# Optimization experiments

Measured on AMD Instinct MI355X. Metric: run time of the kernel, lower is better.

## Reference

```python
import jax, jax.numpy as jnp
import numpy as np

B, L, T_ENC = 64, 128, 256
C_IN, UNITS, OUT = 256, 512, 128  # state_size == motor_size == UNITS (fully-connected wiring)


def _make_params(key):
    ks = jax.random.split(key, 12)
    def rn(k, shape):
        return jax.random.normal(k, shape, dtype=jnp.float32) / np.sqrt(shape[-1])
    cat = C_IN + UNITS  # CfC cell concatenates [input, hx]
    p = {}
    p["W_dec"] = rn(ks[0], (UNITS, 2 * UNITS))                 # fcn_dec, no bias
    p["W_enc"] = rn(ks[1], (UNITS, UNITS)); p["b_enc"] = jnp.zeros((UNITS,), jnp.float32)
    p["w_score"] = rn(ks[2], (1, UNITS))                       # fcn_score Linear(H,1,bias=False)
    p["W_yattn"] = rn(ks[3], (C_IN, UNITS + C_IN)); p["b_yattn"] = jnp.zeros((C_IN,), jnp.float32)
    p["W_ih"] = rn(ks[4], (4 * UNITS, C_IN)); p["b_ih"] = jnp.zeros((4 * UNITS,), jnp.float32)
    p["W_hh"] = rn(ks[5], (4 * UNITS, UNITS))                  # ncps LSTMCell recurrent map has no bias
    p["W_ff1"] = rn(ks[6], (UNITS, cat)); p["b_ff1"] = jnp.zeros((UNITS,), jnp.float32)
    p["W_ff2"] = rn(ks[7], (UNITS, cat)); p["b_ff2"] = jnp.zeros((UNITS,), jnp.float32)
    p["W_ta"] = rn(ks[8], (UNITS, cat)); p["b_ta"] = jnp.zeros((UNITS,), jnp.float32)
    p["W_tb"] = rn(ks[9], (UNITS, cat)); p["b_tb"] = jnp.zeros((UNITS,), jnp.float32)
    p["W_o1"] = rn(ks[10], (UNITS, 2 * UNITS)); p["b_o1"] = jnp.zeros((UNITS,), jnp.float32)
    p["W_o2"] = rn(ks[11], (OUT, UNITS)); p["b_o2"] = jnp.zeros((OUT,), jnp.float32)
    return p


def setup_inputs() -> dict:
    key = jax.random.key(0)
    k1, k2, k3 = jax.random.split(key, 3)
    inp = {
        "x": jax.random.normal(k1, (B, L, C_IN), dtype=jnp.float32),
        "h_en": jax.random.normal(k2, (B, T_ENC, UNITS), dtype=jnp.float32),
    }
    inp.update(_make_params(k3))
    return inp


def _forward(x, h_en, W_dec, W_enc, b_enc, w_score, W_yattn, b_yattn,
             W_ih, b_ih, W_hh, W_ff1, b_ff1, W_ff2, b_ff2,
             W_ta, b_ta, W_tb, b_tb, W_o1, b_o1, W_o2, b_o2):
    Bsz = x.shape[0]
    # fcn_enc applied once outside the time loop (as in the source)
    proj_enc = jnp.einsum('btm,hm->bth', h_en, W_enc) + b_enc  # (B,T_enc,H)
    ts = 1.0  # timespans=None

    def step(carry, xt):
        h, cst, _, _ = carry
        # attention over encoder states
        proj_dec = jnp.concatenate([h, cst], axis=1) @ W_dec.T               # (B,H)
        e = jnp.einsum('bth,h->bt', jnp.tanh(proj_dec[:, None, :] + proj_enc), w_score[0])
        score = jax.nn.softmax(e, axis=1)                                    # softmax over T_enc
        c = jnp.einsum('bt,btm->bm', score, h_en)                            # context (B,M)
        x_hat = jnp.concatenate([xt, c], axis=1) @ W_yattn.T + b_yattn       # (B,C_IN)
        # ncps LSTMCell (forget-gate bias +1)
        z = x_hat @ W_ih.T + b_ih + h @ W_hh.T
        i_, ig, fg, og = jnp.split(z, 4, axis=1)
        new_c = cst * jax.nn.sigmoid(fg + 1.0) + jnp.tanh(i_) * jax.nn.sigmoid(ig)
        h_lstm = jnp.tanh(new_c) * jax.nn.sigmoid(og)
        # WiredCfCCell: single fully-connected layer, mode='default', no backbone
        xx = jnp.concatenate([x_hat, h_lstm], axis=1)                        # (B,C_IN+H)
        ff1 = jnp.tanh(xx @ W_ff1.T + b_ff1)
        ff2 = jnp.tanh(xx @ W_ff2.T + b_ff2)
        t_interp = jax.nn.sigmoid((xx @ W_ta.T + b_ta) * ts + (xx @ W_tb.T + b_tb))
        new_h = ff1 * (1.0 - t_interp) + t_interp * ff2                      # new h_state == h_out
        return (new_h, new_c, new_h, c), None

    h0 = jnp.zeros((Bsz, UNITS), x.dtype)
    init = (h0, h0, h0, jnp.zeros((Bsz, UNITS), x.dtype))
    (h_state, c_state, h_out, c_last), _ = jax.lax.scan(step, init, jnp.swapaxes(x, 0, 1))
    hid = jax.nn.leaky_relu(jnp.concatenate([h_out, c_last], axis=1) @ W_o1.T + b_o1)
    out = hid @ W_o2.T + b_o2
    return out, h_state, c_state


def reference(x, h_en, W_dec, W_enc, b_enc, w_score, W_yattn, b_yattn,
              W_ih, b_ih, W_hh, W_ff1, b_ff1, W_ff2, b_ff2,
              W_ta, b_ta, W_tb, b_tb, W_o1, b_o1, W_o2, b_o2):
    return _forward(x, h_en, W_dec, W_enc, b_enc, w_score, W_yattn, b_yattn,
                    W_ih, b_ih, W_hh, W_ff1, b_ff1, W_ff2, b_ff2,
                    W_ta, b_ta, W_tb, b_tb, W_o1, b_o1, W_o2, b_o2)
```

## Files before the change

### kernel.cpp

```cpp
#include <hip/hip_runtime.h>


constexpr int BSZ  = 64;
constexpr int LSEQ = 128;
constexpr int TENC = 256;
constexpr int CIN  = 256;
constexpr int HU   = 512;
constexpr int ODIM = 128;
constexpr int NBLK = 256;
constexpr int KBIG = 1 << 30;

typedef unsigned long long ull;

struct Params {
  const float *x, *h_en, *W_dec, *W_enc, *b_enc, *w_score, *W_yattn, *b_yattn;
  const float *W_ih, *b_ih, *W_hh;
  const float *W_ff1, *b_ff1, *W_ff2, *b_ff2, *W_ta, *b_ta, *W_tb, *b_tb;
  const float *W_o1, *b_o1, *W_o2, *b_o2;
  float *out;
  float *pe;
  float *pd_part;
  float *e_buf;
  float *ctx;
  float *xhat;
  float *hlstm;
  float *h_buf;
  float *c_buf;
  float *hid;
  unsigned *bar;
  unsigned *flags;
};

__device__ __forceinline__ float frcp_(float x) { return __builtin_amdgcn_rcpf(x); }
__device__ __forceinline__ float ftanh_(float x) {
  return 1.0f - 2.0f * frcp_(1.0f + __expf(2.0f * x));
}
__device__ __forceinline__ float fsig_(float x) {
  return frcp_(1.0f + __expf(-x));
}

__device__ __forceinline__ float ld_c(const float* p) {
  return __hip_atomic_load(p, __ATOMIC_RELAXED, __HIP_MEMORY_SCOPE_AGENT);
}
__device__ __forceinline__ float2 ld_c2(const float* p) {
  union { ull u; float2 f; } c;
  c.u = __hip_atomic_load((const ull*)p, __ATOMIC_RELAXED, __HIP_MEMORY_SCOPE_AGENT);
  return c.f;
}
__device__ __forceinline__ void st_c(float* p, float v) {
  __hip_atomic_store(p, v, __ATOMIC_RELAXED, __HIP_MEMORY_SCOPE_AGENT);
}

__device__ __forceinline__ void gridbar(unsigned* bar, unsigned* flags, unsigned gen) {
  __syncthreads();
  const int t = threadIdx.x;
  if (t == 0) {
    asm volatile("s_waitcnt vmcnt(0) lgkmcnt(0)" ::: "memory");
    __hip_atomic_store(flags + blockIdx.x * 16, gen,
                       __ATOMIC_RELAXED, __HIP_MEMORY_SCOPE_AGENT);
  }
  if (blockIdx.x == 0) {
    while (__hip_atomic_load(flags + t * 16, __ATOMIC_RELAXED,
                             __HIP_MEMORY_SCOPE_AGENT) < gen)
      __builtin_amdgcn_s_sleep(1);
    __syncthreads();
    if (t == 0)
      __hip_atomic_store(bar, gen, __ATOMIC_RELAXED, __HIP_MEMORY_SCOPE_AGENT);
  }
  if (t == 0) {
    while (__hip_atomic_load(bar, __ATOMIC_RELAXED,
                             __HIP_MEMORY_SCOPE_AGENT) < gen)
      __builtin_amdgcn_s_sleep(1);
  }
  __syncthreads();
}

__device__ __forceinline__ void stage128(
    float (*As)[132], float (*Ws)[132], int arows, int wrows,
    const float* const* wr0, const float* const* wr1, int splitW,
    const float* A0, int lda0, bool s0,
    const float* A1, int lda1, bool s1, int splitA, int kb)
{
  const int t = threadIdx.x;
  const float* A; int lda; bool sc;
  if (kb < splitA) { A = A0 + kb;            lda = lda0; sc = s0; }
  else             { A = A1 + (kb - splitA); lda = lda1; sc = s1; }
  if (sc) {
    for (int idx = t; idx < arows * 64; idx += 256) {
      int r = idx >> 6, kd = (idx & 63) << 1;
      *(float2*)&As[r][kd] = ld_c2(A + r * lda + kd);
    }
  } else {
    for (int idx = t; idx < arows * 32; idx += 256) {
      int r = idx >> 5, kq = (idx & 31) << 2;
      *(float4*)&As[r][kq] = *(const float4*)(A + r * lda + kq);
    }
  }
  const float* const* wr; int ko;
  if (kb < splitW) { wr = wr0; ko = kb; } else { wr = wr1; ko = kb - splitW; }
  for (int idx = t; idx < wrows * 32; idx += 256) {
    int c = idx >> 5, kq = (idx & 31) << 2;
    *(float4*)&Ws[c][kq] = *(const float4*)(wr[c] + ko + kq);
  }
}

__device__ __forceinline__ void gemm64x16(
    float (*As)[132], float (*Ws)[132],
    const float* const* wr0, const float* const* wr1, int splitW, const float* biasS,
    const float* A0, int lda0, bool s0, const float* A1, int lda1, bool s1, int splitA,
    int kbase, int klen, float (&acc)[2][2], int& b0o, int& c0o)
{
  const int t = threadIdx.x;
  const int c0 = (t & 7) * 2;
  const int b0 = (t >> 3) * 2;
  __syncthreads();
  acc[0][0] = biasS[c0]; acc[0][1] = biasS[c0 + 1];
  acc[1][0] = biasS[c0]; acc[1][1] = biasS[c0 + 1];
  const int ns = klen >> 7;
  for (int s = 0; s < ns; ++s) {
    stage128(As, Ws, 64, 16, wr0, wr1, splitW, A0, lda0, s0, A1, lda1, s1, splitA,
             kbase + (s << 7));
    __syncthreads();
#pragma unroll
    for (int k4 = 0; k4 < 32; ++k4) {
      float4 w0 = *(float4*)&Ws[c0][k4 << 2];
      float4 w1 = *(float4*)&Ws[c0 + 1][k4 << 2];
#pragma unroll
      for (int i = 0; i < 2; ++i) {
        float4 a = *(float4*)&As[b0 + i][k4 << 2];
        acc[i][0] = fmaf(a.x, w0.x, acc[i][0]);
        acc[i][0] = fmaf(a.y, w0.y, acc[i][0]);
        acc[i][0] = fmaf(a.z, w0.z, acc[i][0]);
        acc[i][0] = fmaf(a.w, w0.w, acc[i][0]);
        acc[i][1] = fmaf(a.x, w1.x, acc[i][1]);
        acc[i][1] = fmaf(a.y, w1.y, acc[i][1]);
        acc[i][1] = fmaf(a.z, w1.z, acc[i][1]);
        acc[i][1] = fmaf(a.w, w1.w, acc[i][1]);
      }
    }
    __syncthreads();
  }
  b0o = b0; c0o = c0;
}

__device__ __forceinline__ void gemm32x16(
    float (*As)[132], float (*Ws)[132],
    const float* const* wr0, const float* const* wr1, int splitW, const float* biasS,
    const float* A0, int lda0, bool s0, const float* A1, int lda1, bool s1, int splitA,
    int kbase, int klen, float (&acc)[2], int& b0o, int& c0o)
{
  const int t = threadIdx.x;
  const int c0 = (t & 7) * 2;
  const int b0 = t >> 3;
  __syncthreads();
  acc[0] = biasS[c0]; acc[1] = biasS[c0 + 1];
  const int ns = klen >> 7;
  for (int s = 0; s < ns; ++s) {
    stage128(As, Ws, 32, 16, wr0, wr1, splitW, A0, lda0, s0, A1, lda1, s1, splitA,
             kbase + (s << 7));
    __syncthreads();
#pragma unroll
    for (int k4 = 0; k4 < 32; ++k4) {
      float4 w0 = *(float4*)&Ws[c0][k4 << 2];
      float4 w1 = *(float4*)&Ws[c0 + 1][k4 << 2];
      float4 a  = *(float4*)&As[b0][k4 << 2];
      acc[0] = fmaf(a.x, w0.x, acc[0]);
      acc[0] = fmaf(a.y, w0.y, acc[0]);
      acc[0] = fmaf(a.z, w0.z, acc[0]);
      acc[0] = fmaf(a.w, w0.w, acc[0]);
      acc[1] = fmaf(a.x, w1.x, acc[1]);
      acc[1] = fmaf(a.y, w1.y, acc[1]);
      acc[1] = fmaf(a.z, w1.z, acc[1]);
      acc[1] = fmaf(a.w, w1.w, acc[1]);
    }
    __syncthreads();
  }
  b0o = b0; c0o = c0;
}

__device__ __forceinline__ void gemm64x32(
    float (*As)[132], float (*Ws)[132],
    const float* const* wr0, const float* biasS,
    const float* A0, int lda0, int klen, float (&acc)[2][4], int& b0o, int& c0o)
{
  const int t = threadIdx.x;
  const int c0 = (t & 7) * 4;
  const int b0 = (t >> 3) * 2;
  __syncthreads();
#pragma unroll
  for (int i = 0; i < 2; ++i)
#pragma unroll
    for (int j = 0; j < 4; ++j) acc[i][j] = biasS[c0 + j];
  const int ns = klen >> 7;
  for (int s = 0; s < ns; ++s) {
    stage128(As, Ws, 64, 32, wr0, wr0, KBIG, A0, lda0, false, A0, lda0, false, KBIG,
             s << 7);
    __syncthreads();
#pragma unroll
    for (int k4 = 0; k4 < 32; ++k4) {
      float4 w0 = *(float4*)&Ws[c0][k4 << 2];
      float4 w1 = *(float4*)&Ws[c0 + 1][k4 << 2];
      float4 w2 = *(float4*)&Ws[c0 + 2][k4 << 2];
      float4 w3 = *(float4*)&Ws[c0 + 3][k4 << 2];
#pragma unroll
      for (int i = 0; i < 2; ++i) {
        float4 a = *(float4*)&As[b0 + i][k4 << 2];
        acc[i][0] = fmaf(a.x, w0.x, acc[i][0]); acc[i][0] = fmaf(a.y, w0.y, acc[i][0]);
        acc[i][0] = fmaf(a.z, w0.z, acc[i][0]); acc[i][0] = fmaf(a.w, w0.w, acc[i][0]);
        acc[i][1] = fmaf(a.x, w1.x, acc[i][1]); acc[i][1] = fmaf(a.y, w1.y, acc[i][1]);
        acc[i][1] = fmaf(a.z, w1.z, acc[i][1]); acc[i][1] = fmaf(a.w, w1.w, acc[i][1]);
        acc[i][2] = fmaf(a.x, w2.x, acc[i][2]); acc[i][2] = fmaf(a.y, w2.y, acc[i][2]);
        acc[i][2] = fmaf(a.z, w2.z, acc[i][2]); acc[i][2] = fmaf(a.w, w2.w, acc[i][2]);
        acc[i][3] = fmaf(a.x, w3.x, acc[i][3]); acc[i][3] = fmaf(a.y, w3.y, acc[i][3]);
        acc[i][3] = fmaf(a.z, w3.z, acc[i][3]); acc[i][3] = fmaf(a.w, w3.w, acc[i][3]);
      }
    }
    __syncthreads();
  }
  b0o = b0; c0o = c0;
}

__launch_bounds__(256)
__global__ void cfc_kernel(Params P) {
  __shared__ float As[64][132];
  __shared__ float Ws[32][132];
  __shared__ const float* wr0[32];
  __shared__ const float* wr1[32];
  __shared__ float biasS[32];
  __shared__ float misc[1088];

  const int t = threadIdx.x;
  unsigned gen = 1;

  for (int job = blockIdx.x; job < 4096 + 32; job += NBLK) {
    if (job < 4096) {
      int rt = job >> 4, ct = job & 15;
      if (t < 32) {
        wr0[t] = P.W_enc + (ct * 32 + t) * HU;
        biasS[t] = P.b_enc[ct * 32 + t];
      }
      float acc[2][4]; int b0, c0;
      gemm64x32(As, Ws, wr0, biasS, P.h_en + rt * 64 * HU, HU, 512, acc, b0, c0);
      float* outp = P.pe + rt * 64 * HU + ct * 32;
#pragma unroll
      for (int i = 0; i < 2; ++i)
#pragma unroll
        for (int j = 0; j < 4; ++j)
          outp[(b0 + i) * HU + c0 + j] = acc[i][j];
    } else {
      int idx = job - 4096;
      float* base = (idx < 16 ? P.h_buf : P.c_buf) + (idx & 15) * 2048;
      for (int i = t; i < 2048; i += 256) st_c(base + i, 0.f);
    }
  }
  __builtin_amdgcn_fence(__ATOMIC_RELEASE, "agent");
  gridbar(P.bar, P.flags, gen++);

  for (int step = 0; step < LSEQ; ++step) {
    const float* xt = P.x + step * CIN;

    {
      int ut = blockIdx.x & 31, ks = blockIdx.x >> 5;
      if (t < 16) {
        wr0[t] = P.W_dec + (ut * 16 + t) * 1024;
        wr1[t] = wr0[t];
        biasS[t] = 0.f;
      }
      float acc[2][2]; int b0, c0;
      gemm64x16(As, Ws, wr0, wr1, KBIG, biasS,
                P.h_buf, HU, true, P.c_buf, HU, true, 512,
                ks * 128, 128, acc, b0, c0);
      float* outp = P.pd_part + ks * (BSZ * HU) + ut * 16;
      st_c(outp + b0 * HU + c0,           acc[0][0]);
      st_c(outp + b0 * HU + c0 + 1,       acc[0][1]);
      st_c(outp + (b0 + 1) * HU + c0,     acc[1][0]);
      st_c(outp + (b0 + 1) * HU + c0 + 1, acc[1][1]);
    }
    gridbar(P.bar, P.flags, gen++);

    {
      int b = blockIdx.x >> 2, tq = blockIdx.x & 3;
      float* pds = misc;
      float* wsc = misc + 520;
      __syncthreads();
      for (int h = t; h < HU; h += 256) {
        float s = 0.f;
#pragma unroll
        for (int p8 = 0; p8 < 8; ++p8) s += ld_c(P.pd_part + p8 * (BSZ * HU) + b * HU + h);
        int hs = h + (h >> 7);
        pds[hs] = s;
        wsc[hs] = P.w_score[h];
      }
      __syncthreads();
      int q = t & 3, tt = tq * 64 + (t >> 2);
      const float* per = P.pe + (b * TENC + tt) * HU + q * 128;
      float acc = 0.f;
      for (int h4 = 0; h4 < 32; ++h4) {
        float4 pv = *(const float4*)(per + h4 * 4);
        int hbs = q * 129 + h4 * 4;
        acc += wsc[hbs + 0] * ftanh_(pds[hbs + 0] + pv.x);
        acc += wsc[hbs + 1] * ftanh_(pds[hbs + 1] + pv.y);
        acc += wsc[hbs + 2] * ftanh_(pds[hbs + 2] + pv.z);
        acc += wsc[hbs + 3] * ftanh_(pds[hbs + 3] + pv.w);
      }
      acc += __shfl_xor(acc, 1);
      acc += __shfl_xor(acc, 2);
      if (q == 0) st_c(P.e_buf + b * TENC + tt, acc);
    }
    gridbar(P.bar, P.flags, gen++);

    {
      int b = blockIdx.x >> 2, mq = blockIdx.x & 3;
      float* es = misc;
      float* red = misc + 512;
      float v = ld_c(P.e_buf + b * TENC + t);
      float m = v;
#pragma unroll
      for (int o = 1; o < 64; o <<= 1) m = fmaxf(m, __shfl_xor(m, o));
      int wid = t >> 6;
      if ((t & 63) == 0) red[wid] = m;
      __syncthreads();
      m = fmaxf(fmaxf(red[0], red[1]), fmaxf(red[2], red[3]));
      float p = __expf(v - m);
      float s = p;
#pragma unroll
      for (int o = 1; o < 64; o <<= 1) s += __shfl_xor(s, o);
      if ((t & 63) == 0) red[4 + wid] = s;
      __syncthreads();
      float sum = (red[4] + red[5]) + (red[6] + red[7]);
      es[t] = p * frcp_(sum);
      __syncthreads();
      if (t < 128) {
        int mcol = mq * 128 + t;
        const float* hb = P.h_en + b * TENC * HU + mcol;
        float a0 = 0.f, a1 = 0.f, a2 = 0.f, a3 = 0.f;
        for (int tt = 0; tt < TENC; tt += 4) {
          a0 = fmaf(es[tt + 0], hb[(tt + 0) * HU], a0);
          a1 = fmaf(es[tt + 1], hb[(tt + 1) * HU], a1);
          a2 = fmaf(es[tt + 2], hb[(tt + 2) * HU], a2);
          a3 = fmaf(es[tt + 3], hb[(tt + 3) * HU], a3);
        }
        st_c(P.ctx + b * HU + mcol, (a0 + a1) + (a2 + a3));
      }
    }
    gridbar(P.bar, P.flags, gen++);

    if (blockIdx.x < 16) {
      int ot = blockIdx.x;
      if (t < 16) {
        wr0[t] = P.W_yattn + (ot * 16 + t) * 768;
        wr1[t] = wr0[t];
        biasS[t] = P.b_yattn[ot * 16 + t];
      }
      float acc[2][2]; int b0, c0;
      gemm64x16(As, Ws, wr0, wr1, KBIG, biasS,
                xt, LSEQ * CIN, false, P.ctx, HU, true, 256,
                0, 768, acc, b0, c0);
      float* outp = P.xhat + ot * 16;
      st_c(outp + b0 * CIN + c0,           acc[0][0]);
      st_c(outp + b0 * CIN + c0 + 1,       acc[0][1]);
      st_c(outp + (b0 + 1) * CIN + c0,     acc[1][0]);
      st_c(outp + (b0 + 1) * CIN + c0 + 1, acc[1][1]);
    }
    gridbar(P.bar, P.flags, gen++);

    {
      int bt = blockIdx.x & 1, jq = blockIdx.x >> 1;
      int j0 = jq * 4, rowbase = bt * 32;
      if (t < 16) {
        int jj = t >> 2, g = t & 3;
        int r = g * 512 + j0 + jj;
        wr0[t] = P.W_ih + r * 256;
        wr1[t] = P.W_hh + r * 512;
        biasS[t] = P.b_ih[r];
      }
      float acc[2]; int b0, c0;
      gemm32x16(As, Ws, wr0, wr1, 256, biasS,
                P.xhat + rowbase * CIN, CIN, true,
                P.h_buf + rowbase * HU, HU, true, 256,
                0, 768, acc, b0, c0);
      float* zs = misc;
      zs[b0 * 16 + c0] = acc[0];
      zs[b0 * 16 + c0 + 1] = acc[1];
      __syncthreads();
      if (t < 128) {
        int b = t >> 2, jj = t & 3;
        int gb = rowbase + b, j = j0 + jj;
        float i_ = zs[b * 16 + jj * 4 + 0];
        float ig = zs[b * 16 + jj * 4 + 1];
        float fg = zs[b * 16 + jj * 4 + 2];
        float og = zs[b * 16 + jj * 4 + 3];
        float cold = ld_c(P.c_buf + gb * HU + j);
        float cn = cold * fsig_(fg + 1.0f) + ftanh_(i_) * fsig_(ig);
        st_c(P.c_buf + gb * HU + j, cn);
        st_c(P.hlstm + gb * HU + j, ftanh_(cn) * fsig_(og));
      }
    }
    gridbar(P.bar, P.flags, gen++);

    {
      int bt = blockIdx.x & 1, jq = blockIdx.x >> 1;
      int j0 = jq * 4, rowbase = bt * 32;
      if (t < 16) {
        int jj = t >> 2, m = t & 3;
        const float* Wm = (m == 0) ? P.W_ff1 : (m == 1) ? P.W_ff2 : (m == 2) ? P.W_ta : P.W_tb;
        const float* bm = (m == 0) ? P.b_ff1 : (m == 1) ? P.b_ff2 : (m == 2) ? P.b_ta : P.b_tb;
        wr0[t] = Wm + (j0 + jj) * 768;
        wr1[t] = wr0[t];
        biasS[t] = bm[j0 + jj];
      }
      float acc[2]; int b0, c0;
      gemm32x16(As, Ws, wr0, wr1, KBIG, biasS,
                P.xhat + rowbase * CIN, CIN, true,
                P.hlstm + rowbase * HU, HU, true, 256,
                0, 768, acc, b0, c0);
      float* es2 = misc;
      es2[b0 * 16 + c0] = acc[0];
      es2[b0 * 16 + c0 + 1] = acc[1];
      __syncthreads();
      if (t < 128) {
        int b = t >> 2, jj = t & 3;
        int gb = rowbase + b, j = j0 + jj;
        float ff1 = ftanh_(es2[b * 16 + jj * 4 + 0]);
        float ff2 = ftanh_(es2[b * 16 + jj * 4 + 1]);
        float ta  = es2[b * 16 + jj * 4 + 2];
        float tb  = es2[b * 16 + jj * 4 + 3];
        float ti = fsig_(ta + tb);
        st_c(P.h_buf + gb * HU + j, ff1 * (1.0f - ti) + ti * ff2);
      }
    }
    gridbar(P.bar, P.flags, gen++);
  }

  if (blockIdx.x < 32) {
    int ut = blockIdx.x;
    if (t < 16) {
      wr0[t] = P.W_o1 + (ut * 16 + t) * 1024;
      wr1[t] = wr0[t];
      biasS[t] = P.b_o1[ut * 16 + t];
    }
    float acc[2][2]; int b0, c0;
    gemm64x16(As, Ws, wr0, wr1, KBIG, biasS,
              P.h_buf, HU, true, P.ctx, HU, true, 512,
              0, 1024, acc, b0, c0);
    float* outp = P.hid + ut * 16;
#pragma unroll
    for (int i = 0; i < 2; ++i)
#pragma unroll
      for (int j = 0; j < 2; ++j) {
        float v = acc[i][j];
        st_c(outp + (b0 + i) * HU + c0 + j, v > 0.f ? v : 0.01f * v);
      }
  }
  gridbar(P.bar, P.flags, gen++);

  {
    int job = blockIdx.x;
    if (job < 8) {
      if (t < 16) {
        wr0[t] = P.W_o2 + (job * 16 + t) * HU;
        wr1[t] = wr0[t];
        biasS[t] = P.b_o2[job * 16 + t];
      }
      float acc[2][2]; int b0, c0;
      gemm64x16(As, Ws, wr0, wr1, KBIG, biasS,
                P.hid, HU, true, P.hid, HU, true, KBIG,
                0, 512, acc, b0, c0);
      float* outp = P.out + job * 16;
      outp[b0 * ODIM + c0] = acc[0][0];
      outp[b0 * ODIM + c0 + 1] = acc[0][1];
      outp[(b0 + 1) * ODIM + c0] = acc[1][0];
      outp[(b0 + 1) * ODIM + c0 + 1] = acc[1][1];
    } else if (job < 40) {
      int idx = job - 8;
      const float* src = (idx < 16 ? P.h_buf : P.c_buf) + (idx & 15) * 2048;
      float* dst = P.out + BSZ * ODIM + (idx < 16 ? 0 : BSZ * HU) + (idx & 15) * 2048;
      for (int i = t; i < 1024; i += 256) {
        float2 f = ld_c2(src + 2 * i);
        *(float2*)(dst + 2 * i) = f;
      }
    }
  }
}

extern "C" void kernel_launch(void* const* d_in, const int* in_sizes, int n_in,
                              void* d_out, int out_size, void* d_ws, size_t ws_size,
                              hipStream_t stream) {
  (void)in_sizes; (void)n_in; (void)out_size; (void)ws_size;
  Params P;
  P.x       = (const float*)d_in[0];
  P.h_en    = (const float*)d_in[1];
  P.W_dec   = (const float*)d_in[2];
  P.W_enc   = (const float*)d_in[3];
  P.b_enc   = (const float*)d_in[4];
  P.w_score = (const float*)d_in[5];
  P.W_yattn = (const float*)d_in[6];
  P.b_yattn = (const float*)d_in[7];
  P.W_ih    = (const float*)d_in[8];
  P.b_ih    = (const float*)d_in[9];
  P.W_hh    = (const float*)d_in[10];
  P.W_ff1   = (const float*)d_in[11];
  P.b_ff1   = (const float*)d_in[12];
  P.W_ff2   = (const float*)d_in[13];
  P.b_ff2   = (const float*)d_in[14];
  P.W_ta    = (const float*)d_in[15];
  P.b_ta    = (const float*)d_in[16];
  P.W_tb    = (const float*)d_in[17];
  P.b_tb    = (const float*)d_in[18];
  P.W_o1    = (const float*)d_in[19];
  P.b_o1    = (const float*)d_in[20];
  P.W_o2    = (const float*)d_in[21];
  P.b_o2    = (const float*)d_in[22];
  P.out     = (float*)d_out;

  float* ws = (float*)d_ws;
  size_t off = 0;
  P.pe      = ws + off; off += (size_t)BSZ * TENC * HU;
  P.pd_part = ws + off; off += (size_t)8 * BSZ * HU;
  P.e_buf   = ws + off; off += (size_t)BSZ * TENC;
  P.ctx     = ws + off; off += (size_t)BSZ * HU;
  P.xhat    = ws + off; off += (size_t)BSZ * CIN;
  P.hlstm   = ws + off; off += (size_t)BSZ * HU;
  P.h_buf   = ws + off; off += (size_t)BSZ * HU;
  P.c_buf   = ws + off; off += (size_t)BSZ * HU;
  P.hid     = ws + off; off += (size_t)BSZ * HU;
  P.bar     = (unsigned*)(ws + off); off += 16;
  P.flags   = (unsigned*)(ws + off);

  (void)hipMemsetAsync((void*)P.bar, 0, 64 + 256 * 64, stream);

  hipLaunchKernelGGL(cfc_kernel, dim3(NBLK), dim3(256), 0, stream, P);
}
```

Before: 17.95 ms.

## Restructure persistent CfC kernel GEMM stages with split-K and more blocks per phase

Replaces the generic staged GEMM helpers with inline LDS tiling and small dot-product microkernels, and splits the y-attention GEMM across K into partial buffers summed by the consumer. Output and head GEMMs now use 32-row batch tiles so more blocks participate. Coherent atomic loads are replaced by plain vector loads, with an acquire fence added after the grid barrier. The encoder-projection job order is also changed. The goal is lower per-step latency in the sequential loop, at the cost of relying on the fence for memory visibility.

```diff
diff --git a/kernel.cpp b/kernel.cpp
--- a/kernel.cpp
+++ b/kernel.cpp
@@ -8,9 +8,6 @@
 constexpr int HU   = 512;
 constexpr int ODIM = 128;
 constexpr int NBLK = 256;
-constexpr int KBIG = 1 << 30;
-
-typedef unsigned long long ull;
 
 struct Params {
   const float *x, *h_en, *W_dec, *W_enc, *b_enc, *w_score, *W_yattn, *b_yattn;
@@ -22,7 +19,7 @@
   float *pd_part;
   float *e_buf;
   float *ctx;
-  float *xhat;
+  float *xh_part;
   float *hlstm;
   float *h_buf;
   float *c_buf;
@@ -39,14 +36,6 @@
   return frcp_(1.0f + __expf(-x));
 }
 
-__device__ __forceinline__ float ld_c(const float* p) {
-  return __hip_atomic_load(p, __ATOMIC_RELAXED, __HIP_MEMORY_SCOPE_AGENT);
-}
-__device__ __forceinline__ float2 ld_c2(const float* p) {
-  union { ull u; float2 f; } c;
-  c.u = __hip_atomic_load((const ull*)p, __ATOMIC_RELAXED, __HIP_MEMORY_SCOPE_AGENT);
-  return c.f;
-}
 __device__ __forceinline__ void st_c(float* p, float v) {
   __hip_atomic_store(p, v, __ATOMIC_RELAXED, __HIP_MEMORY_SCOPE_AGENT);
 }
@@ -71,177 +60,115 @@
     while (__hip_atomic_load(bar, __ATOMIC_RELAXED,
                              __HIP_MEMORY_SCOPE_AGENT) < gen)
       __builtin_amdgcn_s_sleep(1);
+    __builtin_amdgcn_fence(__ATOMIC_ACQUIRE, "agent");
   }
   __syncthreads();
 }
 
-__device__ __forceinline__ void stage128(
-    float (*As)[132], float (*Ws)[132], int arows, int wrows,
-    const float* const* wr0, const float* const* wr1, int splitW,
-    const float* A0, int lda0, bool s0,
-    const float* A1, int lda1, bool s1, int splitA, int kb)
-{
-  const int t = threadIdx.x;
-  const float* A; int lda; bool sc;
-  if (kb < splitA) { A = A0 + kb;            lda = lda0; sc = s0; }
-  else             { A = A1 + (kb - splitA); lda = lda1; sc = s1; }
-  if (sc) {
-    for (int idx = t; idx < arows * 64; idx += 256) {
-      int r = idx >> 6, kd = (idx & 63) << 1;
-      *(float2*)&As[r][kd] = ld_c2(A + r * lda + kd);
-    }
-  } else {
-    for (int idx = t; idx < arows * 32; idx += 256) {
-      int r = idx >> 5, kq = (idx & 31) << 2;
-      *(float4*)&As[r][kq] = *(const float4*)(A + r * lda + kq);
-    }
-  }
-  const float* const* wr; int ko;
-  if (kb < splitW) { wr = wr0; ko = kb; } else { wr = wr1; ko = kb - splitW; }
-  for (int idx = t; idx < wrows * 32; idx += 256) {
-    int c = idx >> 5, kq = (idx & 31) << 2;
-    *(float4*)&Ws[c][kq] = *(const float4*)(wr[c] + ko + kq);
-  }
-}
-
-__device__ __forceinline__ void gemm64x16(
-    float (*As)[132], float (*Ws)[132],
-    const float* const* wr0, const float* const* wr1, int splitW, const float* biasS,
-    const float* A0, int lda0, bool s0, const float* A1, int lda1, bool s1, int splitA,
-    int kbase, int klen, float (&acc)[2][2], int& b0o, int& c0o)
-{
-  const int t = threadIdx.x;
-  const int c0 = (t & 7) * 2;
-  const int b0 = (t >> 3) * 2;
-  __syncthreads();
-  acc[0][0] = biasS[c0]; acc[0][1] = biasS[c0 + 1];
-  acc[1][0] = biasS[c0]; acc[1][1] = biasS[c0 + 1];
-  const int ns = klen >> 7;
-  for (int s = 0; s < ns; ++s) {
-    stage128(As, Ws, 64, 16, wr0, wr1, splitW, A0, lda0, s0, A1, lda1, s1, splitA,
-             kbase + (s << 7));
-    __syncthreads();
-#pragma unroll
-    for (int k4 = 0; k4 < 32; ++k4) {
-      float4 w0 = *(float4*)&Ws[c0][k4 << 2];
-      float4 w1 = *(float4*)&Ws[c0 + 1][k4 << 2];
-#pragma unroll
-      for (int i = 0; i < 2; ++i) {
-        float4 a = *(float4*)&As[b0 + i][k4 << 2];
-        acc[i][0] = fmaf(a.x, w0.x, acc[i][0]);
-        acc[i][0] = fmaf(a.y, w0.y, acc[i][0]);
-        acc[i][0] = fmaf(a.z, w0.z, acc[i][0]);
-        acc[i][0] = fmaf(a.w, w0.w, acc[i][0]);
-        acc[i][1] = fmaf(a.x, w1.x, acc[i][1]);
-        acc[i][1] = fmaf(a.y, w1.y, acc[i][1]);
-        acc[i][1] = fmaf(a.z, w1.z, acc[i][1]);
-        acc[i][1] = fmaf(a.w, w1.w, acc[i][1]);
-      }
-    }
-    __syncthreads();
-  }
-  b0o = b0; c0o = c0;
-}
-
-__device__ __forceinline__ void gemm32x16(
-    float (*As)[132], float (*Ws)[132],
-    const float* const* wr0, const float* const* wr1, int splitW, const float* biasS,
-    const float* A0, int lda0, bool s0, const float* A1, int lda1, bool s1, int splitA,
-    int kbase, int klen, float (&acc)[2], int& b0o, int& c0o)
-{
-  const int t = threadIdx.x;
-  const int c0 = (t & 7) * 2;
-  const int b0 = t >> 3;
-  __syncthreads();
-  acc[0] = biasS[c0]; acc[1] = biasS[c0 + 1];
-  const int ns = klen >> 7;
-  for (int s = 0; s < ns; ++s) {
-    stage128(As, Ws, 32, 16, wr0, wr1, splitW, A0, lda0, s0, A1, lda1, s1, splitA,
-             kbase + (s << 7));
-    __syncthreads();
-#pragma unroll
-    for (int k4 = 0; k4 < 32; ++k4) {
-      float4 w0 = *(float4*)&Ws[c0][k4 << 2];
-      float4 w1 = *(float4*)&Ws[c0 + 1][k4 << 2];
-      float4 a  = *(float4*)&As[b0][k4 << 2];
-      acc[0] = fmaf(a.x, w0.x, acc[0]);
-      acc[0] = fmaf(a.y, w0.y, acc[0]);
-      acc[0] = fmaf(a.z, w0.z, acc[0]);
-      acc[0] = fmaf(a.w, w0.w, acc[0]);
-      acc[1] = fmaf(a.x, w1.x, acc[1]);
-      acc[1] = fmaf(a.y, w1.y, acc[1]);
-      acc[1] = fmaf(a.z, w1.z, acc[1]);
-      acc[1] = fmaf(a.w, w1.w, acc[1]);
-    }
-    __syncthreads();
-  }
-  b0o = b0; c0o = c0;
-}
-
-__device__ __forceinline__ void gemm64x32(
-    float (*As)[132], float (*Ws)[132],
-    const float* const* wr0, const float* biasS,
-    const float* A0, int lda0, int klen, float (&acc)[2][4], int& b0o, int& c0o)
-{
-  const int t = threadIdx.x;
-  const int c0 = (t & 7) * 4;
-  const int b0 = (t >> 3) * 2;
-  __syncthreads();
-#pragma unroll
-  for (int i = 0; i < 2; ++i)
-#pragma unroll
-    for (int j = 0; j < 4; ++j) acc[i][j] = biasS[c0 + j];
-  const int ns = klen >> 7;
-  for (int s = 0; s < ns; ++s) {
-    stage128(As, Ws, 64, 32, wr0, wr0, KBIG, A0, lda0, false, A0, lda0, false, KBIG,
-             s << 7);
-    __syncthreads();
-#pragma unroll
-    for (int k4 = 0; k4 < 32; ++k4) {
-      float4 w0 = *(float4*)&Ws[c0][k4 << 2];
-      float4 w1 = *(float4*)&Ws[c0 + 1][k4 << 2];
-      float4 w2 = *(float4*)&Ws[c0 + 2][k4 << 2];
-      float4 w3 = *(float4*)&Ws[c0 + 3][k4 << 2];
-#pragma unroll
-      for (int i = 0; i < 2; ++i) {
-        float4 a = *(float4*)&As[b0 + i][k4 << 2];
-        acc[i][0] = fmaf(a.x, w0.x, acc[i][0]); acc[i][0] = fmaf(a.y, w0.y, acc[i][0]);
-        acc[i][0] = fmaf(a.z, w0.z, acc[i][0]); acc[i][0] = fmaf(a.w, w0.w, acc[i][0]);
-        acc[i][1] = fmaf(a.x, w1.x, acc[i][1]); acc[i][1] = fmaf(a.y, w1.y, acc[i][1]);
-        acc[i][1] = fmaf(a.z, w1.z, acc[i][1]); acc[i][1] = fmaf(a.w, w1.w, acc[i][1]);
-        acc[i][2] = fmaf(a.x, w2.x, acc[i][2]); acc[i][2] = fmaf(a.y, w2.y, acc[i][2]);
-        acc[i][2] = fmaf(a.z, w2.z, acc[i][2]); acc[i][2] = fmaf(a.w, w2.w, acc[i][2]);
-        acc[i][3] = fmaf(a.x, w3.x, acc[i][3]); acc[i][3] = fmaf(a.y, w3.y, acc[i][3]);
-        acc[i][3] = fmaf(a.z, w3.z, acc[i][3]); acc[i][3] = fmaf(a.w, w3.w, acc[i][3]);
-      }
-    }
-    __syncthreads();
-  }
-  b0o = b0; c0o = c0;
+__device__ __forceinline__ void dot2x2(const float* A0, const float* A1,
+                                       const float* W0, const float* W1,
+                                       int nk4, float (&acc)[2][2]) {
+#pragma unroll 8
+  for (int k4 = 0; k4 < nk4; ++k4) {
+    float4 w0 = *(const float4*)(W0 + (k4 << 2));
+    float4 w1 = *(const float4*)(W1 + (k4 << 2));
+    float4 a0 = *(const float4*)(A0 + (k4 << 2));
+    float4 a1 = *(const float4*)(A1 + (k4 << 2));
+    acc[0][0] = fmaf(a0.x, w0.x, acc[0][0]); acc[0][0] = fmaf(a0.y, w0.y, acc[0][0]);
+    acc[0][0] = fmaf(a0.z, w0.z, acc[0][0]); acc[0][0] = fmaf(a0.w, w0.w, acc[0][0]);
+    acc[0][1] = fmaf(a0.x, w1.x, acc[0][1]); acc[0][1] = fmaf(a0.y, w1.y, acc[0][1]);
+    acc[0][1] = fmaf(a0.z, w1.z, acc[0][1]); acc[0][1] = fmaf(a0.w, w1.w, acc[0][1]);
+    acc[1][0] = fmaf(a1.x, w0.x, acc[1][0]); acc[1][0] = fmaf(a1.y, w0.y, acc[1][0]);
+    acc[1][0] = fmaf(a1.z, w0.z, acc[1][0]); acc[1][0] = fmaf(a1.w, w0.w, acc[1][0]);
+    acc[1][1] = fmaf(a1.x, w1.x, acc[1][1]); acc[1][1] = fmaf(a1.y, w1.y, acc[1][1]);
+    acc[1][1] = fmaf(a1.z, w1.z, acc[1][1]); acc[1][1] = fmaf(a1.w, w1.w, acc[1][1]);
+  }
+}
+
+__device__ __forceinline__ void dot1x2(const float* A0,
+                                       const float* W0, const float* W1,
+                                       int nk4, float (&acc)[2]) {
+#pragma unroll 8
+  for (int k4 = 0; k4 < nk4; ++k4) {
+    float4 w0 = *(const float4*)(W0 + (k4 << 2));
+    float4 w1 = *(const float4*)(W1 + (k4 << 2));
+    float4 a  = *(const float4*)(A0 + (k4 << 2));
+    acc[0] = fmaf(a.x, w0.x, acc[0]); acc[0] = fmaf(a.y, w0.y, acc[0]);
+    acc[0] = fmaf(a.z, w0.z, acc[0]); acc[0] = fmaf(a.w, w0.w, acc[0]);
+    acc[1] = fmaf(a.x, w1.x, acc[1]); acc[1] = fmaf(a.y, w1.y, acc[1]);
+    acc[1] = fmaf(a.z, w1.z, acc[1]); acc[1] = fmaf(a.w, w1.w, acc[1]);
+  }
+}
+
+__device__ __forceinline__ void dot2x4(const float* A0, const float* A1,
+                                       const float* W0, const float* W1,
+                                       const float* W2, const float* W3,
+                                       int nk4, float (&acc)[2][4]) {
+#pragma unroll 4
+  for (int k4 = 0; k4 < nk4; ++k4) {
+    float4 w0 = *(const float4*)(W0 + (k4 << 2));
+    float4 w1 = *(const float4*)(W1 + (k4 << 2));
+    float4 w2 = *(const float4*)(W2 + (k4 << 2));
+    float4 w3 = *(const float4*)(W3 + (k4 << 2));
+#pragma unroll
+    for (int i = 0; i < 2; ++i) {
+      float4 a = *(const float4*)((i ? A1 : A0) + (k4 << 2));
+      acc[i][0] = fmaf(a.x, w0.x, acc[i][0]); acc[i][0] = fmaf(a.y, w0.y, acc[i][0]);
+      acc[i][0] = fmaf(a.z, w0.z, acc[i][0]); acc[i][0] = fmaf(a.w, w0.w, acc[i][0]);
+      acc[i][1] = fmaf(a.x, w1.x, acc[i][1]); acc[i][1] = fmaf(a.y, w1.y, acc[i][1]);
+      acc[i][1] = fmaf(a.z, w1.z, acc[i][1]); acc[i][1] = fmaf(a.w, w1.w, acc[i][1]);
+      acc[i][2] = fmaf(a.x, w2.x, acc[i][2]); acc[i][2] = fmaf(a.y, w2.y, acc[i][2]);
+      acc[i][2] = fmaf(a.z, w2.z, acc[i][2]); acc[i][2] = fmaf(a.w, w2.w, acc[i][2]);
+      acc[i][3] = fmaf(a.x, w3.x, acc[i][3]); acc[i][3] = fmaf(a.y, w3.y, acc[i][3]);
+      acc[i][3] = fmaf(a.z, w3.z, acc[i][3]); acc[i][3] = fmaf(a.w, w3.w, acc[i][3]);
+    }
+  }
 }
 
 __launch_bounds__(256)
 __global__ void cfc_kernel(Params P) {
-  __shared__ float As[64][132];
-  __shared__ float Ws[32][132];
-  __shared__ const float* wr0[32];
-  __shared__ const float* wr1[32];
+  __shared__ float lds[12800];
+  __shared__ const float* wrA[32];
+  __shared__ const float* wrB[32];
   __shared__ float biasS[32];
-  __shared__ float misc[1088];
 
   const int t = threadIdx.x;
   unsigned gen = 1;
 
   for (int job = blockIdx.x; job < 4096 + 32; job += NBLK) {
     if (job < 4096) {
-      int rt = job >> 4, ct = job & 15;
+      int rt = job & 255, ct = job >> 8;
       if (t < 32) {
-        wr0[t] = P.W_enc + (ct * 32 + t) * HU;
+        wrA[t] = P.W_enc + (ct * 32 + t) * HU;
         biasS[t] = P.b_enc[ct * 32 + t];
       }
-      float acc[2][4]; int b0, c0;
-      gemm64x32(As, Ws, wr0, biasS, P.h_en + rt * 64 * HU, HU, 512, acc, b0, c0);
-      float* outp = P.pe + rt * 64 * HU + ct * 32;
+      const int c0 = (t & 7) * 4, b0 = (t >> 3) * 2;
+      __syncthreads();
+      float acc[2][4];
+#pragma unroll
+      for (int i = 0; i < 2; ++i)
+#pragma unroll
+        for (int j = 0; j < 4; ++j) acc[i][j] = biasS[c0 + j];
+      const float* Ab = P.h_en + (size_t)(rt * 64) * HU;
+      for (int s = 0; s < 4; ++s) {
+        int ko = s * 128;
+        for (int idx = t; idx < 2048; idx += 256) {
+          int r = idx >> 5, c4 = idx & 31;
+          *(float4*)&lds[r * 132 + (c4 << 2)] =
+            *(const float4*)(Ab + (size_t)r * HU + ko + (c4 << 2));
+        }
+        for (int idx = t; idx < 1024; idx += 256) {
+          int r = idx >> 5, c4 = idx & 31;
+          *(float4*)&lds[8448 + r * 132 + (c4 << 2)] =
+            *(const float4*)(wrA[r] + ko + (c4 << 2));
+        }
+        __syncthreads();
+        dot2x4(&lds[b0 * 132], &lds[(b0 + 1) * 132],
+               &lds[8448 + c0 * 132], &lds[8448 + (c0 + 1) * 132],
+               &lds[8448 + (c0 + 2) * 132], &lds[8448 + (c0 + 3) * 132], 32, acc);
+        __syncthreads();
+      }
+      float* outp = P.pe + (size_t)(rt * 64) * HU + ct * 32;
 #pragma unroll
       for (int i = 0; i < 2; ++i)
 #pragma unroll
@@ -257,19 +184,27 @@
   gridbar(P.bar, P.flags, gen++);
 
   for (int step = 0; step < LSEQ; ++step) {
-    const float* xt = P.x + step * CIN;
 
     {
       int ut = blockIdx.x & 31, ks = blockIdx.x >> 5;
-      if (t < 16) {
-        wr0[t] = P.W_dec + (ut * 16 + t) * 1024;
-        wr1[t] = wr0[t];
-        biasS[t] = 0.f;
-      }
-      float acc[2][2]; int b0, c0;
-      gemm64x16(As, Ws, wr0, wr1, KBIG, biasS,
-                P.h_buf, HU, true, P.c_buf, HU, true, 512,
-                ks * 128, 128, acc, b0, c0);
+      if (t < 16) wrA[t] = P.W_dec + (ut * 16 + t) * 1024 + ks * 128;
+      const int c0 = (t & 7) * 2, b0 = (t >> 3) * 2;
+      const float* Asrc = (ks < 4) ? (P.h_buf + ks * 128) : (P.c_buf + (ks - 4) * 128);
+      __syncthreads();
+      float acc[2][2] = {{0.f, 0.f}, {0.f, 0.f}};
+      for (int idx = t; idx < 2048; idx += 256) {
+        int r = idx >> 5, c4 = idx & 31;
+        *(float4*)&lds[r * 132 + (c4 << 2)] =
+          *(const float4*)(Asrc + r * HU + (c4 << 2));
+      }
+      for (int idx = t; idx < 512; idx += 256) {
+        int r = idx >> 5, c4 = idx & 31;
+        *(float4*)&lds[8448 + r * 132 + (c4 << 2)] =
+          *(const float4*)(wrA[r] + (c4 << 2));
+      }
+      __syncthreads();
+      dot2x2(&lds[b0 * 132], &lds[(b0 + 1) * 132],
+             &lds[8448 + c0 * 132], &lds[8448 + (c0 + 1) * 132], 32, acc);
       float* outp = P.pd_part + ks * (BSZ * HU) + ut * 16;
       st_c(outp + b0 * HU + c0,           acc[0][0]);
       st_c(outp + b0 * HU + c0 + 1,       acc[0][1]);
@@ -280,28 +215,35 @@
 
     {
       int b = blockIdx.x >> 2, tq = blockIdx.x & 3;
-      float* pds = misc;
-      float* wsc = misc + 520;
-      __syncthreads();
-      for (int h = t; h < HU; h += 256) {
-        float s = 0.f;
-#pragma unroll
-        for (int p8 = 0; p8 < 8; ++p8) s += ld_c(P.pd_part + p8 * (BSZ * HU) + b * HU + h);
+      float* pds = lds;
+      float* wsc = lds + 520;
+      __syncthreads();
+      {
+        int h = t * 2;
+        float sx = 0.f, sy = 0.f;
+#pragma unroll
+        for (int p8 = 0; p8 < 8; ++p8) {
+          float2 v = *(const float2*)(P.pd_part + p8 * (BSZ * HU) + b * HU + h);
+          sx += v.x; sy += v.y;
+        }
         int hs = h + (h >> 7);
-        pds[hs] = s;
-        wsc[hs] = P.w_score[h];
+        pds[hs] = sx; pds[hs + 1] = sy;
+        float2 w = *(const float2*)(P.w_score + h);
+        wsc[hs] = w.x; wsc[hs + 1] = w.y;
       }
       __syncthreads();
       int q = t & 3, tt = tq * 64 + (t >> 2);
-      const float* per = P.pe + (b * TENC + tt) * HU + q * 128;
+      const float* per = P.pe + (size_t)(b * TENC + tt) * HU + q * 128;
+      const float* pd = pds + q * 129;
+      const float* wv = wsc + q * 129;
       float acc = 0.f;
       for (int h4 = 0; h4 < 32; ++h4) {
-        float4 pv = *(const float4*)(per + h4 * 4);
-        int hbs = q * 129 + h4 * 4;
-        acc += wsc[hbs + 0] * ftanh_(pds[hbs + 0] + pv.x);
-        acc += wsc[hbs + 1] * ftanh_(pds[hbs + 1] + pv.y);
-        acc += wsc[hbs + 2] * ftanh_(pds[hbs + 2] + pv.z);
-        acc += wsc[hbs + 3] * ftanh_(pds[hbs + 3] + pv.w);
+        float4 pv = *(const float4*)(per + (h4 << 2));
+        int o = h4 << 2;
+        acc += wv[o + 0] * ftanh_(pd[o + 0] + pv.x);
+        acc += wv[o + 1] * ftanh_(pd[o + 1] + pv.y);
+        acc += wv[o + 2] * ftanh_(pd[o + 2] + pv.z);
+        acc += wv[o + 3] * ftanh_(pd[o + 3] + pv.w);
       }
       acc += __shfl_xor(acc, 1);
       acc += __shfl_xor(acc, 2);
@@ -311,9 +253,9 @@
 
     {
       int b = blockIdx.x >> 2, mq = blockIdx.x & 3;
-      float* es = misc;
-      float* red = misc + 512;
-      float v = ld_c(P.e_buf + b * TENC + t);
+      float* es = lds;
+      float* red = lds + 260;
+      float v = P.e_buf[b * TENC + t];
       float m = v;
 #pragma unroll
       for (int o = 1; o < 64; o <<= 1) m = fmaxf(m, __shfl_xor(m, o));
@@ -332,7 +274,7 @@
       __syncthreads();
       if (t < 128) {
         int mcol = mq * 128 + t;
-        const float* hb = P.h_en + b * TENC * HU + mcol;
+        const float* hb = P.h_en + (size_t)b * TENC * HU + mcol;
         float a0 = 0.f, a1 = 0.f, a2 = 0.f, a3 = 0.f;
         for (int tt = 0; tt < TENC; tt += 4) {
           a0 = fmaf(es[tt + 0], hb[(tt + 0) * HU], a0);
@@ -345,18 +287,37 @@
     }
     gridbar(P.bar, P.flags, gen++);
 
-    if (blockIdx.x < 16) {
-      int ot = blockIdx.x;
+    if (blockIdx.x < 32) {
+      int ct = blockIdx.x & 15, ks = blockIdx.x >> 4;
       if (t < 16) {
-        wr0[t] = P.W_yattn + (ot * 16 + t) * 768;
-        wr1[t] = wr0[t];
-        biasS[t] = P.b_yattn[ot * 16 + t];
-      }
-      float acc[2][2]; int b0, c0;
-      gemm64x16(As, Ws, wr0, wr1, KBIG, biasS,
-                xt, LSEQ * CIN, false, P.ctx, HU, true, 256,
-                0, 768, acc, b0, c0);
-      float* outp = P.xhat + ot * 16;
+        wrA[t] = P.W_yattn + (ct * 16 + t) * 768 + ks * 384;
+        biasS[t] = ks ? 0.f : P.b_yattn[ct * 16 + t];
+      }
+      const int c0 = (t & 7) * 2, b0 = (t >> 3) * 2;
+      __syncthreads();
+      float acc[2][2];
+      acc[0][0] = biasS[c0]; acc[0][1] = biasS[c0 + 1];
+      acc[1][0] = biasS[c0]; acc[1][1] = biasS[c0 + 1];
+      for (int s = 0; s < 3; ++s) {
+        int k = ks * 384 + s * 128;
+        for (int idx = t; idx < 2048; idx += 256) {
+          int r = idx >> 5, c4 = idx & 31;
+          const float* src = (k < 256)
+            ? (P.x + ((size_t)r * LSEQ + step) * CIN + k)
+            : (P.ctx + r * HU + (k - 256));
+          *(float4*)&lds[r * 132 + (c4 << 2)] = *(const float4*)(src + (c4 << 2));
+        }
+        for (int idx = t; idx < 512; idx += 256) {
+          int r = idx >> 5, c4 = idx & 31;
+          *(float4*)&lds[8448 + r * 132 + (c4 << 2)] =
+            *(const float4*)(wrA[r] + s * 128 + (c4 << 2));
+        }
+        __syncthreads();
+        dot2x2(&lds[b0 * 132], &lds[(b0 + 1) * 132],
+               &lds[8448 + c0 * 132], &lds[8448 + (c0 + 1) * 132], 32, acc);
+        __syncthreads();
+      }
+      float* outp = P.xh_part + ks * (BSZ * CIN) + ct * 16;
       st_c(outp + b0 * CIN + c0,           acc[0][0]);
       st_c(outp + b0 * CIN + c0 + 1,       acc[0][1]);
       st_c(outp + (b0 + 1) * CIN + c0,     acc[1][0]);
@@ -370,27 +331,57 @@
       if (t < 16) {
         int jj = t >> 2, g = t & 3;
         int r = g * 512 + j0 + jj;
-        wr0[t] = P.W_ih + r * 256;
-        wr1[t] = P.W_hh + r * 512;
+        wrA[t] = P.W_ih + r * 256;
+        wrB[t] = P.W_hh + (size_t)r * 512;
         biasS[t] = P.b_ih[r];
       }
-      float acc[2]; int b0, c0;
-      gemm32x16(As, Ws, wr0, wr1, 256, biasS,
-                P.xhat + rowbase * CIN, CIN, true,
-                P.h_buf + rowbase * HU, HU, true, 256,
-                0, 768, acc, b0, c0);
-      float* zs = misc;
+      const int c0 = (t & 7) * 2, b0 = t >> 3;
+      __syncthreads();
+      float acc[2];
+      acc[0] = biasS[c0]; acc[1] = biasS[c0 + 1];
+      for (int s = 0; s < 3; ++s) {
+        if (s == 0) {
+          for (int idx = t; idx < 2048; idx += 256) {
+            int r = idx >> 6, c4 = idx & 63; int gb = rowbase + r;
+            float4 a = *(const float4*)(P.xh_part + gb * CIN + (c4 << 2));
+            float4 b2 = *(const float4*)(P.xh_part + BSZ * CIN + gb * CIN + (c4 << 2));
+            a.x += b2.x; a.y += b2.y; a.z += b2.z; a.w += b2.w;
+            *(float4*)&lds[r * 260 + (c4 << 2)] = a;
+          }
+          for (int idx = t; idx < 1024; idx += 256) {
+            int r = idx >> 6, c4 = idx & 63;
+            *(float4*)&lds[8320 + r * 260 + (c4 << 2)] =
+              *(const float4*)(wrA[r] + (c4 << 2));
+          }
+        } else {
+          int ho = (s - 1) * 256;
+          for (int idx = t; idx < 2048; idx += 256) {
+            int r = idx >> 6, c4 = idx & 63; int gb = rowbase + r;
+            *(float4*)&lds[r * 260 + (c4 << 2)] =
+              *(const float4*)(P.h_buf + gb * HU + ho + (c4 << 2));
+          }
+          for (int idx = t; idx < 1024; idx += 256) {
+            int r = idx >> 6, c4 = idx & 63;
+            *(float4*)&lds[8320 + r * 260 + (c4 << 2)] =
+              *(const float4*)(wrB[r] + ho + (c4 << 2));
+          }
+        }
+        __syncthreads();
+        dot1x2(&lds[b0 * 260], &lds[8320 + c0 * 260], &lds[8320 + (c0 + 1) * 260], 64, acc);
+        __syncthreads();
+      }
+      float* zs = lds;
       zs[b0 * 16 + c0] = acc[0];
       zs[b0 * 16 + c0 + 1] = acc[1];
       __syncthreads();
       if (t < 128) {
-        int b = t >> 2, jj = t & 3;
-        int gb = rowbase + b, j = j0 + jj;
-        float i_ = zs[b * 16 + jj * 4 + 0];
-        float ig = zs[b * 16 + jj * 4 + 1];
-        float fg = zs[b * 16 + jj * 4 + 2];
-        float og = zs[b * 16 + jj * 4 + 3];
-        float cold = ld_c(P.c_buf + gb * HU + j);
+        int b2 = t >> 2, jj = t & 3;
+        int gb = rowbase + b2, j = j0 + jj;
+        float i_ = zs[b2 * 16 + jj * 4 + 0];
+        float ig = zs[b2 * 16 + jj * 4 + 1];
+        float fg = zs[b2 * 16 + jj * 4 + 2];
+        float og = zs[b2 * 16 + jj * 4 + 3];
+        float cold = P.c_buf[gb * HU + j];
         float cn = cold * fsig_(fg + 1.0f) + ftanh_(i_) * fsig_(ig);
         st_c(P.c_buf + gb * HU + j, cn);
         st_c(P.hlstm + gb * HU + j, ftanh_(cn) * fsig_(og));
@@ -405,26 +396,50 @@
         int jj = t >> 2, m = t & 3;
         const float* Wm = (m == 0) ? P.W_ff1 : (m == 1) ? P.W_ff2 : (m == 2) ? P.W_ta : P.W_tb;
         const float* bm = (m == 0) ? P.b_ff1 : (m == 1) ? P.b_ff2 : (m == 2) ? P.b_ta : P.b_tb;
-        wr0[t] = Wm + (j0 + jj) * 768;
-        wr1[t] = wr0[t];
+        wrA[t] = Wm + (j0 + jj) * 768;
         biasS[t] = bm[j0 + jj];
       }
-      float acc[2]; int b0, c0;
-      gemm32x16(As, Ws, wr0, wr1, KBIG, biasS,
-                P.xhat + rowbase * CIN, CIN, true,
-                P.hlstm + rowbase * HU, HU, true, 256,
-                0, 768, acc, b0, c0);
-      float* es2 = misc;
+      const int c0 = (t & 7) * 2, b0 = t >> 3;
+      __syncthreads();
+      float acc[2];
+      acc[0] = biasS[c0]; acc[1] = biasS[c0 + 1];
+      for (int s = 0; s < 3; ++s) {
+        if (s == 0) {
+          for (int idx = t; idx < 2048; idx += 256) {
+            int r = idx >> 6, c4 = idx & 63; int gb = rowbase + r;
+            float4 a = *(const float4*)(P.xh_part + gb * CIN + (c4 << 2));
+            float4 b2 = *(const float4*)(P.xh_part + BSZ * CIN + gb * CIN + (c4 << 2));
+            a.x += b2.x; a.y += b2.y; a.z += b2.z; a.w += b2.w;
+            *(float4*)&lds[r * 260 + (c4 << 2)] = a;
+          }
+        } else {
+          int ho = (s - 1) * 256;
+          for (int idx = t; idx < 2048; idx += 256) {
+            int r = idx >> 6, c4 = idx & 63; int gb = rowbase + r;
+            *(float4*)&lds[r * 260 + (c4 << 2)] =
+              *(const float4*)(P.hlstm + gb * HU + ho + (c4 << 2));
+          }
+        }
+        for (int idx = t; idx < 1024; idx += 256) {
+          int r = idx >> 6, c4 = idx & 63;
+          *(float4*)&lds[8320 + r * 260 + (c4 << 2)] =
+            *(const float4*)(wrA[r] + s * 256 + (c4 << 2));
+        }
+        __syncthreads();
+        dot1x2(&lds[b0 * 260], &lds[8320 + c0 * 260], &lds[8320 + (c0 + 1) * 260], 64, acc);
+        __syncthreads();
+      }
+      float* es2 = lds;
       es2[b0 * 16 + c0] = acc[0];
       es2[b0 * 16 + c0 + 1] = acc[1];
       __syncthreads();
       if (t < 128) {
-        int b = t >> 2, jj = t & 3;
-        int gb = rowbase + b, j = j0 + jj;
-        float ff1 = ftanh_(es2[b * 16 + jj * 4 + 0]);
-        float ff2 = ftanh_(es2[b * 16 + jj * 4 + 1]);
-        float ta  = es2[b * 16 + jj * 4 + 2];
-        float tb  = es2[b * 16 + jj * 4 + 3];
+        int b2 = t >> 2, jj = t & 3;
+        int gb = rowbase + b2, j = j0 + jj;
+        float ff1 = ftanh_(es2[b2 * 16 + jj * 4 + 0]);
+        float ff2 = ftanh_(es2[b2 * 16 + jj * 4 + 1]);
+        float ta  = es2[b2 * 16 + jj * 4 + 2];
+        float tb  = es2[b2 * 16 + jj * 4 + 3];
         float ti = fsig_(ta + tb);
         st_c(P.h_buf + gb * HU + j, ff1 * (1.0f - ti) + ti * ff2);
       }
@@ -432,53 +447,76 @@
     gridbar(P.bar, P.flags, gen++);
   }
 
-  if (blockIdx.x < 32) {
-    int ut = blockIdx.x;
+  if (blockIdx.x < 64) {
+    int bt = blockIdx.x & 1, ut = blockIdx.x >> 1;
+    int rowbase = bt * 32;
     if (t < 16) {
-      wr0[t] = P.W_o1 + (ut * 16 + t) * 1024;
-      wr1[t] = wr0[t];
+      wrA[t] = P.W_o1 + (ut * 16 + t) * 1024;
       biasS[t] = P.b_o1[ut * 16 + t];
     }
-    float acc[2][2]; int b0, c0;
-    gemm64x16(As, Ws, wr0, wr1, KBIG, biasS,
-              P.h_buf, HU, true, P.ctx, HU, true, 512,
-              0, 1024, acc, b0, c0);
-    float* outp = P.hid + ut * 16;
-#pragma unroll
-    for (int i = 0; i < 2; ++i)
-#pragma unroll
-      for (int j = 0; j < 2; ++j) {
-        float v = acc[i][j];
-        st_c(outp + (b0 + i) * HU + c0 + j, v > 0.f ? v : 0.01f * v);
-      }
+    const int c0 = (t & 7) * 2, b0 = t >> 3;
+    __syncthreads();
+    float acc[2];
+    acc[0] = biasS[c0]; acc[1] = biasS[c0 + 1];
+    for (int s = 0; s < 4; ++s) {
+      const float* src = (s < 2) ? (P.h_buf + s * 256) : (P.ctx + (s - 2) * 256);
+      for (int idx = t; idx < 2048; idx += 256) {
+        int r = idx >> 6, c4 = idx & 63; int gb = rowbase + r;
+        *(float4*)&lds[r * 260 + (c4 << 2)] = *(const float4*)(src + gb * HU + (c4 << 2));
+      }
+      for (int idx = t; idx < 1024; idx += 256) {
+        int r = idx >> 6, c4 = idx & 63;
+        *(float4*)&lds[8320 + r * 260 + (c4 << 2)] =
+          *(const float4*)(wrA[r] + s * 256 + (c4 << 2));
+      }
+      __syncthreads();
+      dot1x2(&lds[b0 * 260], &lds[8320 + c0 * 260], &lds[8320 + (c0 + 1) * 260], 64, acc);
+      __syncthreads();
+    }
+#pragma unroll
+    for (int j = 0; j < 2; ++j) {
+      float v = acc[j];
+      st_c(P.hid + (rowbase + b0) * HU + ut * 16 + c0 + j, v > 0.f ? v : 0.01f * v);
+    }
   }
   gridbar(P.bar, P.flags, gen++);
 
   {
     int job = blockIdx.x;
-    if (job < 8) {
+    if (job < 16) {
+      int bt = job & 1, ot = job >> 1;
+      int rowbase = bt * 32;
       if (t < 16) {
-        wr0[t] = P.W_o2 + (job * 16 + t) * HU;
-        wr1[t] = wr0[t];
-        biasS[t] = P.b_o2[job * 16 + t];
-      }
-      float acc[2][2]; int b0, c0;
-      gemm64x16(As, Ws, wr0, wr1, KBIG, biasS,
-                P.hid, HU, true, P.hid, HU, true, KBIG,
-                0, 512, acc, b0, c0);
-      float* outp = P.out + job * 16;
-      outp[b0 * ODIM + c0] = acc[0][0];
-      outp[b0 * ODIM + c0 + 1] = acc[0][1];
-      outp[(b0 + 1) * ODIM + c0] = acc[1][0];
-      outp[(b0 + 1) * ODIM + c0 + 1] = acc[1][1];
-    } else if (job < 40) {
-      int idx = job - 8;
+        wrA[t] = P.W_o2 + (ot * 16 + t) * HU;
+        biasS[t] = P.b_o2[ot * 16 + t];
+      }
+      const int c0 = (t & 7) * 2, b0 = t >> 3;
+      __syncthreads();
+      float acc[2];
+      acc[0] = biasS[c0]; acc[1] = biasS[c0 + 1];
+      for (int s = 0; s < 2; ++s) {
+        for (int idx = t; idx < 2048; idx += 256) {
+          int r = idx >> 6, c4 = idx & 63; int gb = rowbase + r;
+          *(float4*)&lds[r * 260 + (c4 << 2)] =
+            *(const float4*)(P.hid + gb * HU + s * 256 + (c4 << 2));
+        }
+        for (int idx = t; idx < 1024; idx += 256) {
+          int r = idx >> 6, c4 = idx & 63;
+          *(float4*)&lds[8320 + r * 260 + (c4 << 2)] =
+            *(const float4*)(wrA[r] + s * 256 + (c4 << 2));
+        }
+        __syncthreads();
+        dot1x2(&lds[b0 * 260], &lds[8320 + c0 * 260], &lds[8320 + (c0 + 1) * 260], 64, acc);
+        __syncthreads();
+      }
+      P.out[(rowbase + b0) * ODIM + ot * 16 + c0]     = acc[0];
+      P.out[(rowbase + b0) * ODIM + ot * 16 + c0 + 1] = acc[1];
+    } else if (job < 48) {
+      int idx = job - 16;
       const float* src = (idx < 16 ? P.h_buf : P.c_buf) + (idx & 15) * 2048;
       float* dst = P.out + BSZ * ODIM + (idx < 16 ? 0 : BSZ * HU) + (idx & 15) * 2048;
-      for (int i = t; i < 1024; i += 256) {
-        float2 f = ld_c2(src + 2 * i);
-        *(float2*)(dst + 2 * i) = f;
-      }
+      for (int i = t; i < 512; i += 256)
+        *(float4*)(dst + 4 * i) = *(const float4*)(src + 4 * i);
     }
   }
 }
@@ -519,7 +557,7 @@
   P.pd_part = ws + off; off += (size_t)8 * BSZ * HU;
   P.e_buf   = ws + off; off += (size_t)BSZ * TENC;
   P.ctx     = ws + off; off += (size_t)BSZ * HU;
-  P.xhat    = ws + off; off += (size_t)BSZ * CIN;
+  P.xh_part = ws + off; off += (size_t)2 * BSZ * CIN;
   P.hlstm   = ws + off; off += (size_t)BSZ * HU;
   P.h_buf   = ws + off; off += (size_t)BSZ * HU;
   P.c_buf   = ws + off; off += (size_t)BSZ * HU;
```

After: 14.44 ms. 19.6% less time.
